# Performance work log

Hardware: AMD Instinct MI355X
Metric: run time of the kernel (lower is better)

The kernel has to match this reference:

```python
import jax, jax.numpy as jnp
import numpy as np

THRESH = 230.0   # options['dist_threshold'][0]
NCAT = 21        # options['supervised_categories']


def setup_inputs() -> dict:
    key = jax.random.key(0)
    k1, k2, k3 = jax.random.split(key, 3)
    b, N, d, T = 8, 16384, 128, 64  # N = h*w = 128*128
    frame_embeddings = jax.random.normal(k1, (b, N, d), dtype=jnp.float32)
    templates = jax.random.normal(k2, (T, N, d), dtype=jnp.float32)
    template_classes = jax.random.randint(k3, (T,), 0, 20, dtype=jnp.int64)
    return {"frame_embeddings": frame_embeddings, "templates": templates,
            "template_classes": template_classes}


def _min_dists(frame_embeddings, templates):
    # frame_embeddings: [b, n, d]; templates: [t, n, d]
    x2 = jnp.sum(frame_embeddings * frame_embeddings, axis=-1)          # [b, n]
    t2 = jnp.sum(templates * templates, axis=-1)                        # [t, n]
    xt = jnp.einsum('bnd,tnd->btn', frame_embeddings, templates)        # [b, t, n]
    dists = x2[:, None, :] - 2.0 * xt + t2[None, :, :]                  # [b, t, n]
    min_d = jnp.min(dists, axis=1)                                      # [b, n]
    min_idx = jnp.argmin(dists, axis=1)                                 # [b, n]
    return min_d, min_idx


def reference(frame_embeddings, templates, template_classes):
    b, N, _ = frame_embeddings.shape
    min_d, min_idx = _min_dists(frame_embeddings, templates)
    neigh_classes = template_classes[min_idx]                           # [b, n]
    mask = min_d <= THRESH                                              # [b, n] bool
    one_hot = jax.nn.one_hot(neigh_classes, NCAT, dtype=jnp.float32)    # [b, n, ncat]
    masked_pred = one_hot * mask[:, :, None].astype(jnp.float32)        # [b, n, ncat]
    neigh_classes_masked = jnp.where(mask, neigh_classes, NCAT - 1)     # [b, n]
    return (masked_pred, mask, neigh_classes_masked, min_d, neigh_classes)
```

## Files before the change

kernel.cpp:

```cpp
#include <hip/hip_runtime.h>


#define NPIX   16384
#define DDIM   128
#define NT     64
#define NB     8
#define NCAT   21
#define THRESH 230.0f
#define P      16

typedef float4 f4;

__device__ __forceinline__ void dma16(const float* g, float* l) {
    __builtin_amdgcn_global_load_lds(
        (const __attribute__((address_space(1))) void*)g,
        (__attribute__((address_space(3))) void*)l,
        16 , 0, 0);
}

__global__ __launch_bounds__(256, 4) void nn_openset_kernel(
    const float* __restrict__ frame,
    const float* __restrict__ tmpl,
    const int*   __restrict__ tcls,
    float* __restrict__ out)
{
    __shared__ __align__(16) float ts[4][P * DDIM];

    const int tid = threadIdx.x;
    const int n0  = blockIdx.x * P;

    const int bp = tid >> 6;
    const int ln = tid & 63;
    const int np = ln >> 2;
    const int dq = ln & 3;
    const int b0 = bp * 2, b1 = b0 + 1;
    const int n  = n0 + np;
    const int wv = __builtin_amdgcn_readfirstlane(bp);

    f4 fr0[8], fr1[8];
    {
        const f4* f0 = (const f4*)(frame + ((size_t)b0 * NPIX + n) * DDIM + dq * 32);
        const f4* f1 = (const f4*)(frame + ((size_t)b1 * NPIX + n) * DDIM + dq * 32);
        #pragma unroll
        for (int j = 0; j < 8; ++j) { fr0[j] = f0[j]; fr1[j] = f1[j]; }
    }

    const size_t PLANE = (size_t)NPIX * DDIM;
    const int c0  = tid;
    const int c1  = tid + 256;
    const int sc0 = c0 ^ ((c0 >> 5) & 7);
    const int sc1 = c1 ^ ((c1 >> 5) & 7);
    const float* gp0 = tmpl + (size_t)n0 * DDIM + sc0 * 4;
    const float* gp1 = tmpl + (size_t)n0 * DDIM + sc1 * 4;
    const int ldso0 = wv * 256;
    const int ldso1 = 1024 + wv * 256;

    dma16(gp0,             &ts[0][ldso0]);  dma16(gp1,             &ts[0][ldso1]);
    dma16(gp0 + PLANE,     &ts[1][ldso0]);  dma16(gp1 + PLANE,     &ts[1][ldso1]);
    dma16(gp0 + 2 * PLANE, &ts[2][ldso0]);  dma16(gp1 + 2 * PLANE, &ts[2][ldso1]);
    gp0 += 3 * PLANE;  gp1 += 3 * PLANE;

    const int s  = np & 7;
    const int rb = np * DDIM + dq * 32;
    int roff[8];
    #pragma unroll
    for (int kq = 0; kq < 8; ++kq) roff[kq] = rb + ((kq ^ s) << 2);

    asm volatile("s_waitcnt vmcnt(4)" ::: "memory");
    __builtin_amdgcn_s_barrier();

    float vmin0 = 3.402823466e38f, vmin1 = 3.402823466e38f;
    int   imin0 = 0, imin1 = 0;

    for (int t = 0; t < NT; ++t) {
        if (t + 3 < NT) {
            float* wb = ts[(t + 3) & 3];
            dma16(gp0, wb + ldso0);
            dma16(gp1, wb + ldso1);
            gp0 += PLANE;  gp1 += PLANE;
        }

        const float* tb = ts[t & 3];
        float a0 = 0.0f, a1 = 0.0f;
        #pragma unroll
        for (int kq = 0; kq < 8; ++kq) {
            const f4 tv = *(const f4*)(tb + roff[kq]);
            const f4 x0 = fr0[kq];
            const f4 x1 = fr1[kq];
            float d;
            d = x0.x - tv.x; a0 = fmaf(d, d, a0);
            d = x0.y - tv.y; a0 = fmaf(d, d, a0);
            d = x0.z - tv.z; a0 = fmaf(d, d, a0);
            d = x0.w - tv.w; a0 = fmaf(d, d, a0);
            d = x1.x - tv.x; a1 = fmaf(d, d, a1);
            d = x1.y - tv.y; a1 = fmaf(d, d, a1);
            d = x1.z - tv.z; a1 = fmaf(d, d, a1);
            d = x1.w - tv.w; a1 = fmaf(d, d, a1);
        }
        a0 += __shfl_xor(a0, 1);  a0 += __shfl_xor(a0, 2);
        a1 += __shfl_xor(a1, 1);  a1 += __shfl_xor(a1, 2);

        const bool u0 = a0 < vmin0;
        const bool u1 = a1 < vmin1;
        imin0 = u0 ? t : imin0;  vmin0 = u0 ? a0 : vmin0;
        imin1 = u1 ? t : imin1;  vmin1 = u1 ? a1 : vmin1;

        if (t < NT - 1) {
            if (t < NT - 3)       asm volatile("s_waitcnt vmcnt(4)" ::: "memory");
            else if (t == NT - 3) asm volatile("s_waitcnt vmcnt(2)" ::: "memory");
            else                  asm volatile("s_waitcnt vmcnt(0)" ::: "memory");
            __builtin_amdgcn_s_barrier();
        }
    }

    const int  cls0 = tcls[imin0];
    const int  cls1 = tcls[imin1];
    const bool m0 = (vmin0 <= THRESH);
    const bool m1 = (vmin1 <= THRESH);

    float* o0 = out;
    float* o1 = out + (size_t)NB * NPIX * NCAT;
    float* o2 = o1 + NB * NPIX;
    float* o3 = o2 + NB * NPIX;
    float* o4 = o3 + NB * NPIX;

    const size_t p0 = (size_t)b0 * NPIX + n;
    const size_t p1 = (size_t)b1 * NPIX + n;

    if (dq == 0)      { o1[p0] = m0 ? 1.0f : 0.0f;          o1[p1] = m1 ? 1.0f : 0.0f; }
    else if (dq == 1) { o2[p0] = m0 ? (float)cls0 : 20.0f;  o2[p1] = m1 ? (float)cls1 : 20.0f; }
    else if (dq == 2) { o3[p0] = vmin0;                     o3[p1] = vmin1; }
    else              { o4[p0] = (float)cls0;               o4[p1] = (float)cls1; }

    #pragma unroll
    for (int j = 0; j < 6; ++j) {
        const int c = dq * 6 + j;
        if (c < NCAT) {
            o0[p0 * NCAT + c] = (m0 && c == cls0) ? 1.0f : 0.0f;
            o0[p1 * NCAT + c] = (m1 && c == cls1) ? 1.0f : 0.0f;
        }
    }
}

extern "C" void kernel_launch(void* const* d_in, const int* in_sizes, int n_in,
                              void* d_out, int out_size, void* d_ws, size_t ws_size,
                              hipStream_t stream) {
    const float* frame = (const float*)d_in[0];
    const float* tmpl  = (const float*)d_in[1];
    const int*   tcls  = (const int*)d_in[2];
    float* outp = (float*)d_out;
    nn_openset_kernel<<<NPIX / P, 256, 0, stream>>>(frame, tmpl, tcls, outp);
}
```

Measured before the change: 717.5 us.

## Give each wave private template tiles and drop block barriers

Each block now covers 8 pixels instead of 16, and each wave handles 2 pixels across all 8 batches. Every wave streams its own template slice into LDS, so the per-iteration workgroup barrier is removed and only per-wave vmcnt waits remain. The cost is twice as many blocks, fewer frame registers per lane, and an extra shuffle step in the reduction, with lane count and read patterns altered to match. Template reuse per block is halved, but waves no longer stall on each other.

```diff
diff --git a/kernel.cpp b/kernel.cpp
--- a/kernel.cpp
+++ b/kernel.cpp
@@ -7,7 +7,6 @@
 #define NB     8
 #define NCAT   21
 #define THRESH 230.0f
-#define P      16
 
 typedef float4 f4;
 
@@ -24,66 +23,52 @@
     const int*   __restrict__ tcls,
     float* __restrict__ out)
 {
-    __shared__ __align__(16) float ts[4][P * DDIM];
+    __shared__ __align__(16) float ts[4][4][256];
 
     const int tid = threadIdx.x;
-    const int n0  = blockIdx.x * P;
+    const int wv  = tid >> 6;
+    const int ln  = tid & 63;
+    const int np  = ln >> 5;
+    const int b   = (ln >> 3) & 3;
+    const int dq8 = ln & 7;
+    const int n   = blockIdx.x * 8 + wv * 2 + np;
+    const int b0  = b, b1 = b + 4;
 
-    const int bp = tid >> 6;
-    const int ln = tid & 63;
-    const int np = ln >> 2;
-    const int dq = ln & 3;
-    const int b0 = bp * 2, b1 = b0 + 1;
-    const int n  = n0 + np;
-    const int wv = __builtin_amdgcn_readfirstlane(bp);
-
-    f4 fr0[8], fr1[8];
+    f4 fr0[4], fr1[4];
     {
-        const f4* f0 = (const f4*)(frame + ((size_t)b0 * NPIX + n) * DDIM + dq * 32);
-        const f4* f1 = (const f4*)(frame + ((size_t)b1 * NPIX + n) * DDIM + dq * 32);
+        const f4* f0 = (const f4*)(frame + ((size_t)b0 * NPIX + n) * DDIM + dq8 * 16);
+        const f4* f1 = (const f4*)(frame + ((size_t)b1 * NPIX + n) * DDIM + dq8 * 16);
         #pragma unroll
-        for (int j = 0; j < 8; ++j) { fr0[j] = f0[j]; fr1[j] = f1[j]; }
+        for (int j = 0; j < 4; ++j) { fr0[j] = f0[j]; fr1[j] = f1[j]; }
     }
 
     const size_t PLANE = (size_t)NPIX * DDIM;
-    const int c0  = tid;
-    const int c1  = tid + 256;
-    const int sc0 = c0 ^ ((c0 >> 5) & 7);
-    const int sc1 = c1 ^ ((c1 >> 5) & 7);
-    const float* gp0 = tmpl + (size_t)n0 * DDIM + sc0 * 4;
-    const float* gp1 = tmpl + (size_t)n0 * DDIM + sc1 * 4;
-    const int ldso0 = wv * 256;
-    const int ldso1 = 1024 + wv * 256;
+    const int sx  = ((ln >> 5) << 2) | ((ln >> 3) & 3);
+    const int src = (ln & ~7) | ((ln & 7) ^ sx);
+    const float* gp = tmpl + (size_t)(blockIdx.x * 8 + wv * 2) * DDIM + src * 4;
 
-    dma16(gp0,             &ts[0][ldso0]);  dma16(gp1,             &ts[0][ldso1]);
-    dma16(gp0 + PLANE,     &ts[1][ldso0]);  dma16(gp1 + PLANE,     &ts[1][ldso1]);
-    dma16(gp0 + 2 * PLANE, &ts[2][ldso0]);  dma16(gp1 + 2 * PLANE, &ts[2][ldso1]);
-    gp0 += 3 * PLANE;  gp1 += 3 * PLANE;
+    const int s3 = (np << 2) | (dq8 >> 1);
+    int roff[4];
+    #pragma unroll
+    for (int kq = 0; kq < 4; ++kq)
+        roff[kq] = np * 128 + (((dq8 * 4 + kq) ^ s3) << 2);
 
-    const int s  = np & 7;
-    const int rb = np * DDIM + dq * 32;
-    int roff[8];
-    #pragma unroll
-    for (int kq = 0; kq < 8; ++kq) roff[kq] = rb + ((kq ^ s) << 2);
-
-    asm volatile("s_waitcnt vmcnt(4)" ::: "memory");
-    __builtin_amdgcn_s_barrier();
+    dma16(gp,             &ts[0][wv][0]);
+    dma16(gp + PLANE,     &ts[1][wv][0]);
+    dma16(gp + 2 * PLANE, &ts[2][wv][0]);
+    gp += 3 * PLANE;
+    asm volatile("s_waitcnt vmcnt(2)" ::: "memory");
 
     float vmin0 = 3.402823466e38f, vmin1 = 3.402823466e38f;
     int   imin0 = 0, imin1 = 0;
 
     for (int t = 0; t < NT; ++t) {
-        if (t + 3 < NT) {
-            float* wb = ts[(t + 3) & 3];
-            dma16(gp0, wb + ldso0);
-            dma16(gp1, wb + ldso1);
-            gp0 += PLANE;  gp1 += PLANE;
-        }
+        if (t + 3 < NT) { dma16(gp, &ts[(t + 3) & 3][wv][0]); gp += PLANE; }
 
-        const float* tb = ts[t & 3];
+        const float* tb = &ts[t & 3][wv][0];
         float a0 = 0.0f, a1 = 0.0f;
         #pragma unroll
-        for (int kq = 0; kq < 8; ++kq) {
+        for (int kq = 0; kq < 4; ++kq) {
             const f4 tv = *(const f4*)(tb + roff[kq]);
             const f4 x0 = fr0[kq];
             const f4 x1 = fr1[kq];
@@ -97,8 +82,8 @@
             d = x1.z - tv.z; a1 = fmaf(d, d, a1);
             d = x1.w - tv.w; a1 = fmaf(d, d, a1);
         }
-        a0 += __shfl_xor(a0, 1);  a0 += __shfl_xor(a0, 2);
-        a1 += __shfl_xor(a1, 1);  a1 += __shfl_xor(a1, 2);
+        a0 += __shfl_xor(a0, 1); a0 += __shfl_xor(a0, 2); a0 += __shfl_xor(a0, 4);
+        a1 += __shfl_xor(a1, 1); a1 += __shfl_xor(a1, 2); a1 += __shfl_xor(a1, 4);
 
         const bool u0 = a0 < vmin0;
         const bool u1 = a1 < vmin1;
@@ -106,10 +91,9 @@
         imin1 = u1 ? t : imin1;  vmin1 = u1 ? a1 : vmin1;
 
         if (t < NT - 1) {
-            if (t < NT - 3)       asm volatile("s_waitcnt vmcnt(4)" ::: "memory");
-            else if (t == NT - 3) asm volatile("s_waitcnt vmcnt(2)" ::: "memory");
+            if (t < NT - 3)       asm volatile("s_waitcnt vmcnt(2)" ::: "memory");
+            else if (t == NT - 3) asm volatile("s_waitcnt vmcnt(1)" ::: "memory");
             else                  asm volatile("s_waitcnt vmcnt(0)" ::: "memory");
-            __builtin_amdgcn_s_barrier();
         }
     }
 
@@ -127,14 +111,14 @@
     const size_t p0 = (size_t)b0 * NPIX + n;
     const size_t p1 = (size_t)b1 * NPIX + n;
 
-    if (dq == 0)      { o1[p0] = m0 ? 1.0f : 0.0f;          o1[p1] = m1 ? 1.0f : 0.0f; }
-    else if (dq == 1) { o2[p0] = m0 ? (float)cls0 : 20.0f;  o2[p1] = m1 ? (float)cls1 : 20.0f; }
-    else if (dq == 2) { o3[p0] = vmin0;                     o3[p1] = vmin1; }
-    else              { o4[p0] = (float)cls0;               o4[p1] = (float)cls1; }
+    if (dq8 == 0)      { o1[p0] = m0 ? 1.0f : 0.0f;          o1[p1] = m1 ? 1.0f : 0.0f; }
+    else if (dq8 == 1) { o2[p0] = m0 ? (float)cls0 : 20.0f;  o2[p1] = m1 ? (float)cls1 : 20.0f; }
+    else if (dq8 == 2) { o3[p0] = vmin0;                     o3[p1] = vmin1; }
+    else if (dq8 == 3) { o4[p0] = (float)cls0;               o4[p1] = (float)cls1; }
 
     #pragma unroll
-    for (int j = 0; j < 6; ++j) {
-        const int c = dq * 6 + j;
+    for (int j = 0; j < 3; ++j) {
+        const int c = dq8 * 3 + j;
         if (c < NCAT) {
             o0[p0 * NCAT + c] = (m0 && c == cls0) ? 1.0f : 0.0f;
             o0[p1 * NCAT + c] = (m1 && c == cls1) ? 1.0f : 0.0f;
@@ -149,5 +133,5 @@
     const float* tmpl  = (const float*)d_in[1];
     const int*   tcls  = (const int*)d_in[2];
     float* outp = (float*)d_out;
-    nn_openset_kernel<<<NPIX / P, 256, 0, stream>>>(frame, tmpl, tcls, outp);
+    nn_openset_kernel<<<NPIX / 8, 256, 0, stream>>>(frame, tmpl, tcls, outp);
 }
```

Measured after the change: 746.0 us. 1.04x slower.
